# Kernel optimization log

Hardware: AMD Instinct MI355X
Metric: run time of the kernel (lower is better)

## Reference

```python
import jax, jax.numpy as jnp
import numpy as np

B, Z, TDIM, CF, A, R, T = 1024, 256, 512, 1024, 64, 128, 64

def _lstm_cell(x, h, c, Wih, Whh, b):
    # PyTorch gate order: i, f, g, o
    g = x @ Wih.T + h @ Whh.T + b
    i, f, gg, o = jnp.split(g, 4, axis=-1)
    c = jax.nn.sigmoid(f) * c + jax.nn.sigmoid(i) * jnp.tanh(gg)
    h = jax.nn.sigmoid(o) * jnp.tanh(c)
    return h, c

def setup_inputs() -> dict:
    key = jax.random.key(0)
    ks = jax.random.split(key, 24)
    s = lambda k, shape, fan: jax.random.normal(k, shape, jnp.float32) * (1.0 / np.sqrt(fan))
    d = {}
    d['z'] = jax.random.normal(ks[0], (B, Z), jnp.float32)
    d['z2t_w'] = s(ks[1], (TDIM, Z), Z)
    d['z2t_b'] = jnp.zeros((TDIM,), jnp.float32)
    in_a, in_r, in_t = TDIM + A, TDIM + A + R, TDIM + A + 1
    d['Wih_a'] = s(ks[2], (4 * CF, in_a), in_a); d['Whh_a'] = s(ks[3], (4 * CF, CF), CF); d['b_a'] = jnp.zeros((4 * CF,), jnp.float32)
    d['Wih_r'] = s(ks[4], (4 * CF, in_r), in_r); d['Whh_r'] = s(ks[5], (4 * CF, CF), CF); d['b_r'] = jnp.zeros((4 * CF,), jnp.float32)
    d['Wih_t'] = s(ks[6], (4 * CF, in_t), in_t); d['Whh_t'] = s(ks[7], (4 * CF, CF), CF); d['b_t'] = jnp.zeros((4 * CF,), jnp.float32)
    d['e2act_w'] = s(ks[8], (A, CF), CF); d['e2act_b'] = jnp.zeros((A,), jnp.float32)
    d['e2res_w'] = s(ks[9], (R, CF), CF); d['e2res_b'] = jnp.zeros((R,), jnp.float32)
    d['e2ts_w1'] = s(ks[10], (CF // 2, CF), CF); d['e2ts_b1'] = jnp.zeros((CF // 2,), jnp.float32)
    d['e2ts_w2'] = s(ks[11], (1, CF // 2), CF // 2); d['e2ts_b2'] = jnp.zeros((1,), jnp.float32)
    return d

def reference(z, z2t_w, z2t_b, Wih_a, Whh_a, b_a, Wih_r, Whh_r, b_r, Wih_t, Whh_t, b_t,
              e2act_w, e2act_b, e2res_w, e2res_b, e2ts_w1, e2ts_b1, e2ts_w2, e2ts_b2):
    t_rec = jax.nn.relu(z @ z2t_w.T + z2t_b)                  # [B, TDIM]
    b = t_rec.shape[0]
    act_oh = jnp.tile(jax.nn.one_hot(A - 1, A, dtype=jnp.float32), (b, 1))   # EOT activity
    res_oh = jnp.tile(jax.nn.one_hot(R - 1, R, dtype=jnp.float32), (b, 1))   # EOT resource
    ts_v = jnp.zeros((b, 1), jnp.float32)
    zeros_h = jnp.zeros((b, CF), jnp.float32)
    carry0 = (act_oh, res_oh, ts_v, zeros_h, zeros_h, zeros_h, zeros_h, zeros_h, zeros_h)

    def step(carry, _):
        act_oh, res_oh, ts_v, ha, ca, hr, cr, ht, ct = carry
        xa = jnp.concatenate([t_rec, act_oh], axis=-1)
        ha, ca = _lstm_cell(xa, ha, ca, Wih_a, Whh_a, b_a)
        act_logits = ha @ e2act_w.T + e2act_b                 # [B, A]
        act_oh2 = jax.nn.one_hot(jnp.argmax(act_logits, axis=-1), A, dtype=jnp.float32)
        xr = jnp.concatenate([t_rec, act_oh2, res_oh], axis=-1)
        hr, cr = _lstm_cell(xr, hr, cr, Wih_r, Whh_r, b_r)
        res_logits = hr @ e2res_w.T + e2res_b                 # [B, R]
        res_oh2 = jax.nn.one_hot(jnp.argmax(res_logits, axis=-1), R, dtype=jnp.float32)
        xt = jnp.concatenate([t_rec, act_oh2, ts_v], axis=-1)
        ht, ct = _lstm_cell(xt, ht, ct, Wih_t, Whh_t, b_t)
        ts_new = jax.nn.relu(ht @ e2ts_w1.T + e2ts_b1) @ e2ts_w2.T + e2ts_b2  # [B, 1]
        new_carry = (act_oh2, res_oh2, ts_new, ha, ca, hr, cr, ht, ct)
        return new_carry, (act_logits, res_logits, ts_new)

    _, (act_seq, res_seq, ts_seq) = jax.lax.scan(step, carry0, None, length=T)
    acts_rec = jax.nn.softmax(jnp.transpose(act_seq, (1, 0, 2)), axis=2)   # [B, T, A]
    ress_rec = jax.nn.softmax(jnp.transpose(res_seq, (1, 0, 2)), axis=2)   # [B, T, R]
    ts_rec = jnp.transpose(ts_seq[..., 0], (1, 0))                         # [B, T]
    return acts_rec, ts_rec, ress_rec
```

## Files before the change

kernel.cpp:

```cpp
#include <hip/hip_runtime.h>
#include <math.h>


__device__ __forceinline__ float sigf(float x) { return 1.0f / (1.0f + expf(-x)); }

typedef __attribute__((ext_vector_type(8))) _Float16 f16x8;
typedef __attribute__((ext_vector_type(4))) float f32x4;

__device__ __forceinline__ void split_f16(float x, unsigned short& hi, unsigned short& lo) {
    _Float16 h = (_Float16)x;
    float r = (x - (float)h) * 2048.0f;
    _Float16 l = (_Float16)r;
    hi = __builtin_bit_cast(unsigned short, h);
    lo = __builtin_bit_cast(unsigned short, l);
}

#define GLDS(gp, lp) __builtin_amdgcn_global_load_lds( \
    (const __attribute__((address_space(1))) void*)(gp), \
    (__attribute__((address_space(3))) void*)(lp), 16, 0, 0)

__global__ __launch_bounds__(256, 4) void step1(
    const unsigned short* __restrict__ Ah, const unsigned short* __restrict__ Al,
    const unsigned short* __restrict__ WA0, const unsigned short* __restrict__ WA1,
    const float* __restrict__ base_a, const float* __restrict__ Ea, const int* __restrict__ aidx,
    float* __restrict__ ca, unsigned short* __restrict__ oAh, unsigned short* __restrict__ oAl,
    float* __restrict__ haf,
    const unsigned short* __restrict__ Th, const unsigned short* __restrict__ Tl,
    const unsigned short* __restrict__ W10, const unsigned short* __restrict__ W11,
    const float* __restrict__ b1, float* __restrict__ u,
    const float* __restrict__ hrf, const float* __restrict__ resT4, const float* __restrict__ resb,
    float* __restrict__ out_res, int* __restrict__ ridx, int t, int Loff)
{
    int L = blockIdx.x + Loff;
    if (L >= 576) {
        if (t == 0) return;
        int lane = threadIdx.x & 63, w = threadIdx.x >> 6;
        int b = (L - 576) * 4 + w;
        float acc0 = resb[lane], acc1 = resb[lane + 64];
        const float4* arow = (const float4*)(hrf + (size_t)b * 1024);
#pragma unroll 4
        for (int k4 = 0; k4 < 256; k4++) {
            float4 a4 = arow[k4];
            float4 w40 = *(const float4*)(resT4 + ((size_t)k4 * 128 + lane) * 4);
            float4 w41 = *(const float4*)(resT4 + ((size_t)k4 * 128 + lane + 64) * 4);
            acc0 += a4.x * w40.x + a4.y * w40.y + a4.z * w40.z + a4.w * w40.w;
            acc1 += a4.x * w41.x + a4.y * w41.y + a4.z * w41.z + a4.w * w41.w;
        }
        float v = acc0; int idx = lane;
        if (acc1 > v) { v = acc1; idx = lane + 64; }
#pragma unroll
        for (int off = 32; off; off >>= 1) {
            float ov = __shfl_xor(v, off);
            int   oi = __shfl_xor(idx, off);
            if (ov > v || (ov == v && oi < idx)) { v = ov; idx = oi; }
        }
        float e0 = expf(acc0 - v), e1 = expf(acc1 - v);
        float s = e0 + e1;
#pragma unroll
        for (int off = 32; off; off >>= 1) s += __shfl_xor(s, off);
        float* dst = out_res + ((size_t)b * 64 + (t - 1)) * 128;
        dst[lane] = e0 / s; dst[lane + 64] = e1 / s;
        if (lane == 0) ridx[b] = idx;
        return;
    }

    __shared__ unsigned short lds[8192];
    const unsigned short *pAh, *pAl, *pWh, *pWl;
    int x, jy; bool isA;
    if (L < 512) {
        isA = true;
        int xcd = L & 7, idx = L >> 3;
        jy = xcd * 8 + (idx >> 3);
        x = idx & 7;
        pAh = Ah; pAl = Al; pWh = WA0; pWl = WA1;
    } else {
        isA = false;
        int t2 = L - 512;
        x = t2 & 7; jy = t2 >> 3;
        pAh = Th; pAl = Tl; pWh = W10; pWl = W11;
    }
    const int tid = threadIdx.x, wave = tid >> 6, lane = tid & 63;
    const int lrow = lane & 15, lq = lane >> 4;
    const int m0 = x * 128;

    f32x4 acch[2][4], accl[2][4];
#pragma unroll
    for (int i = 0; i < 2; i++)
#pragma unroll
        for (int j = 0; j < 4; j++) {
            acch[i][j] = (f32x4){0.f, 0.f, 0.f, 0.f};
            accl[i][j] = (f32x4){0.f, 0.f, 0.f, 0.f};
        }

    const int nrow = isA ? (wave * 1024 + jy * 16 + lrow) : (jy * 64 + wave * 16 + lrow);
    const size_t ar0 = (size_t)(m0 + (wave * 2 + 0) * 16 + lrow) * 1024 + lq * 8;
    const size_t ar1 = (size_t)(m0 + (wave * 2 + 1) * 16 + lrow) * 1024 + lq * 8;

    f16x8 ah[2][2], al[2][2];

    auto LOADA = [&](int it, int s) {
        int k = it * 32;
        ah[s][0] = *(const f16x8*)(pAh + ar0 + k);
        al[s][0] = *(const f16x8*)(pAl + ar0 + k);
        ah[s][1] = *(const f16x8*)(pAh + ar1 + k);
        al[s][1] = *(const f16x8*)(pAl + ar1 + k);
    };
    auto STAGEB = [&](int it, int p) {
        int k = it * 32 + lq * 8;
        unsigned short* bp = &lds[p * 4096];
        GLDS(pWh + (size_t)nrow * 1024 + k, bp + wave * 512);
        GLDS(pWl + (size_t)nrow * 1024 + k, bp + 2048 + wave * 512);
    };
    auto COMPUTE = [&](int s, int p) {
        unsigned short* bp = &lds[p * 4096];
#pragma unroll
        for (int nh = 0; nh < 2; nh++) {
            f16x8 bh[2], bl[2];
#pragma unroll
            for (int q = 0; q < 2; q++) {
                int ni = nh * 2 + q;
                bh[q] = *(const f16x8*)(bp + ni * 512 + lane * 8);
                bl[q] = *(const f16x8*)(bp + 2048 + ni * 512 + lane * 8);
            }
#pragma unroll
            for (int mi = 0; mi < 2; mi++)
#pragma unroll
                for (int q = 0; q < 2; q++) {
                    int ni = nh * 2 + q;
                    acch[mi][ni] = __builtin_amdgcn_mfma_f32_16x16x32_f16(ah[s][mi], bh[q], acch[mi][ni], 0, 0, 0);
                    accl[mi][ni] = __builtin_amdgcn_mfma_f32_16x16x32_f16(al[s][mi], bh[q], accl[mi][ni], 0, 0, 0);
                    accl[mi][ni] = __builtin_amdgcn_mfma_f32_16x16x32_f16(ah[s][mi], bl[q], accl[mi][ni], 0, 0, 0);
                }
        }
    };

    LOADA(0, 0);
    STAGEB(0, 0);
    for (int it = 0; it < 30; it += 2) {
        STAGEB(it + 1, 1);
        asm volatile("s_waitcnt vmcnt(2)" ::: "memory");
        __builtin_amdgcn_s_barrier();
        __builtin_amdgcn_sched_barrier(0);
        LOADA(it + 1, 1);
        COMPUTE(0, 0);
        __builtin_amdgcn_sched_barrier(0);
        __builtin_amdgcn_s_barrier();
        STAGEB(it + 2, 0);
        asm volatile("s_waitcnt vmcnt(2)" ::: "memory");
        __builtin_amdgcn_s_barrier();
        __builtin_amdgcn_sched_barrier(0);
        LOADA(it + 2, 0);
        COMPUTE(1, 1);
        __builtin_amdgcn_sched_barrier(0);
        __builtin_amdgcn_s_barrier();
    }
    STAGEB(31, 1);
    asm volatile("s_waitcnt vmcnt(2)" ::: "memory");
    __builtin_amdgcn_s_barrier();
    __builtin_amdgcn_sched_barrier(0);
    LOADA(31, 1);
    COMPUTE(0, 0);
    __builtin_amdgcn_sched_barrier(0);
    __builtin_amdgcn_s_barrier();
    asm volatile("s_waitcnt vmcnt(0)" ::: "memory");
    __builtin_amdgcn_s_barrier();
    __builtin_amdgcn_sched_barrier(0);
    COMPUTE(1, 1);

    const float s_lo = 1.0f / 2048.0f;
    if (isA) {
        int j = jy * 16 + lrow;
#pragma unroll
        for (int mi = 0; mi < 2; mi++)
#pragma unroll
            for (int r = 0; r < 4; r++) {
                int row = m0 + wave * 32 + mi * 16 + lq * 4 + r;
                size_t rb = (size_t)row * 4096 + j;
                const float* e1 = Ea + (size_t)aidx[row] * 4096 + j;
                float gi = acch[mi][0][r] + accl[mi][0][r] * s_lo + base_a[rb]        + e1[0];
                float gf = acch[mi][1][r] + accl[mi][1][r] * s_lo + base_a[rb + 1024] + e1[1024];
                float gg = acch[mi][2][r] + accl[mi][2][r] * s_lo + base_a[rb + 2048] + e1[2048];
                float go = acch[mi][3][r] + accl[mi][3][r] * s_lo + base_a[rb + 3072] + e1[3072];
                size_t ci = (size_t)row * 1024 + j;
                float cn = sigf(gf) * ca[ci] + sigf(gi) * tanhf(gg);
                ca[ci] = cn;
                float hn = sigf(go) * tanhf(cn);
                haf[ci] = hn;
                split_f16(hn, oAh[ci], oAl[ci]);
            }
    } else {
#pragma unroll
        for (int mi = 0; mi < 2; mi++)
#pragma unroll
            for (int ni = 0; ni < 4; ni++) {
                int col = jy * 64 + ni * 16 + lrow;
                float bv = b1[col];
#pragma unroll
                for (int r = 0; r < 4; r++) {
                    int row = m0 + wave * 32 + mi * 16 + lq * 4 + r;
                    float v = acch[mi][ni][r] + accl[mi][ni][r] * s_lo + bv;
                    u[(size_t)row * 512 + col] = fmaxf(v, 0.0f);
                }
            }
    }
}

__global__ __launch_bounds__(256, 4) void step3(
    const unsigned short* __restrict__ Rh, const unsigned short* __restrict__ Rl,
    const unsigned short* __restrict__ WR0, const unsigned short* __restrict__ WR1,
    const float* __restrict__ base_r, const float* __restrict__ Er_a, const float* __restrict__ Er_r,
    const int* __restrict__ aidx, const int* __restrict__ ridx, const float* __restrict__ tsv,
    float* __restrict__ cr, unsigned short* __restrict__ oRh, unsigned short* __restrict__ oRl,
    float* __restrict__ hrf,
    const unsigned short* __restrict__ Th, const unsigned short* __restrict__ Tl,
    const unsigned short* __restrict__ WT0, const unsigned short* __restrict__ WT1,
    const float* __restrict__ base_t, const float* __restrict__ Et_a, const float* __restrict__ wtts,
    float* __restrict__ ct, unsigned short* __restrict__ oTh, unsigned short* __restrict__ oTl)
{
    __shared__ unsigned short lds[8192];
    int L = blockIdx.x;
    int xcd = L & 7, idx = L >> 3;
    int g = xcd * 16 + (idx >> 3);
    int x = idx & 7;
    int z = g >> 6, jy = g & 63;
    const unsigned short* pAh = z ? Th : Rh;
    const unsigned short* pAl = z ? Tl : Rl;
    const unsigned short* pWh = z ? WT0 : WR0;
    const unsigned short* pWl = z ? WT1 : WR1;

    const int tid = threadIdx.x, wave = tid >> 6, lane = tid & 63;
    const int lrow = lane & 15, lq = lane >> 4;
    const int m0 = x * 128;

    f32x4 acch[2][4], accl[2][4];
#pragma unroll
    for (int i = 0; i < 2; i++)
#pragma unroll
        for (int j = 0; j < 4; j++) {
            acch[i][j] = (f32x4){0.f, 0.f, 0.f, 0.f};
            accl[i][j] = (f32x4){0.f, 0.f, 0.f, 0.f};
        }

    const int nrow = wave * 1024 + jy * 16 + lrow;
    const size_t ar0 = (size_t)(m0 + (wave * 2 + 0) * 16 + lrow) * 1024 + lq * 8;
    const size_t ar1 = (size_t)(m0 + (wave * 2 + 1) * 16 + lrow) * 1024 + lq * 8;

    f16x8 ah[2][2], al[2][2];

    auto LOADA = [&](int it, int s) {
        int k = it * 32;
        ah[s][0] = *(const f16x8*)(pAh + ar0 + k);
        al[s][0] = *(const f16x8*)(pAl + ar0 + k);
        ah[s][1] = *(const f16x8*)(pAh + ar1 + k);
        al[s][1] = *(const f16x8*)(pAl + ar1 + k);
    };
    auto STAGEB = [&](int it, int p) {
        int k = it * 32 + lq * 8;
        unsigned short* bp = &lds[p * 4096];
        GLDS(pWh + (size_t)nrow * 1024 + k, bp + wave * 512);
        GLDS(pWl + (size_t)nrow * 1024 + k, bp + 2048 + wave * 512);
    };
    auto COMPUTE = [&](int s, int p) {
        unsigned short* bp = &lds[p * 4096];
#pragma unroll
        for (int nh = 0; nh < 2; nh++) {
            f16x8 bh[2], bl[2];
#pragma unroll
            for (int q = 0; q < 2; q++) {
                int ni = nh * 2 + q;
                bh[q] = *(const f16x8*)(bp + ni * 512 + lane * 8);
                bl[q] = *(const f16x8*)(bp + 2048 + ni * 512 + lane * 8);
            }
#pragma unroll
            for (int mi = 0; mi < 2; mi++)
#pragma unroll
                for (int q = 0; q < 2; q++) {
                    int ni = nh * 2 + q;
                    acch[mi][ni] = __builtin_amdgcn_mfma_f32_16x16x32_f16(ah[s][mi], bh[q], acch[mi][ni], 0, 0, 0);
                    accl[mi][ni] = __builtin_amdgcn_mfma_f32_16x16x32_f16(al[s][mi], bh[q], accl[mi][ni], 0, 0, 0);
                    accl[mi][ni] = __builtin_amdgcn_mfma_f32_16x16x32_f16(ah[s][mi], bl[q], accl[mi][ni], 0, 0, 0);
                }
        }
    };

    LOADA(0, 0);
    STAGEB(0, 0);
    for (int it = 0; it < 30; it += 2) {
        STAGEB(it + 1, 1);
        asm volatile("s_waitcnt vmcnt(2)" ::: "memory");
        __builtin_amdgcn_s_barrier();
        __builtin_amdgcn_sched_barrier(0);
        LOADA(it + 1, 1);
        COMPUTE(0, 0);
        __builtin_amdgcn_sched_barrier(0);
        __builtin_amdgcn_s_barrier();
        STAGEB(it + 2, 0);
        asm volatile("s_waitcnt vmcnt(2)" ::: "memory");
        __builtin_amdgcn_s_barrier();
        __builtin_amdgcn_sched_barrier(0);
        LOADA(it + 2, 0);
        COMPUTE(1, 1);
        __builtin_amdgcn_sched_barrier(0);
        __builtin_amdgcn_s_barrier();
    }
    STAGEB(31, 1);
    asm volatile("s_waitcnt vmcnt(2)" ::: "memory");
    __builtin_amdgcn_s_barrier();
    __builtin_amdgcn_sched_barrier(0);
    LOADA(31, 1);
    COMPUTE(0, 0);
    __builtin_amdgcn_sched_barrier(0);
    __builtin_amdgcn_s_barrier();
    asm volatile("s_waitcnt vmcnt(0)" ::: "memory");
    __builtin_amdgcn_s_barrier();
    __builtin_amdgcn_sched_barrier(0);
    COMPUTE(1, 1);

    const float s_lo = 1.0f / 2048.0f;
    const int j = jy * 16 + lrow;
    if (z == 0) {
#pragma unroll
        for (int mi = 0; mi < 2; mi++)
#pragma unroll
            for (int r = 0; r < 4; r++) {
                int row = m0 + wave * 32 + mi * 16 + lq * 4 + r;
                size_t rb = (size_t)row * 4096 + j;
                const float* e1 = Er_a + (size_t)aidx[row] * 4096 + j;
                const float* e2 = Er_r + (size_t)ridx[row] * 4096 + j;
                float gi = acch[mi][0][r] + accl[mi][0][r] * s_lo + base_r[rb]        + e1[0]    + e2[0];
                float gf = acch[mi][1][r] + accl[mi][1][r] * s_lo + base_r[rb + 1024] + e1[1024] + e2[1024];
                float gg = acch[mi][2][r] + accl[mi][2][r] * s_lo + base_r[rb + 2048] + e1[2048] + e2[2048];
                float go = acch[mi][3][r] + accl[mi][3][r] * s_lo + base_r[rb + 3072] + e1[3072] + e2[3072];
                size_t ci = (size_t)row * 1024 + j;
                float cn = sigf(gf) * cr[ci] + sigf(gi) * tanhf(gg);
                cr[ci] = cn;
                float hn = sigf(go) * tanhf(cn);
                hrf[ci] = hn;
                split_f16(hn, oRh[ci], oRl[ci]);
            }
    } else {
#pragma unroll
        for (int mi = 0; mi < 2; mi++)
#pragma unroll
            for (int r = 0; r < 4; r++) {
                int row = m0 + wave * 32 + mi * 16 + lq * 4 + r;
                size_t rb = (size_t)row * 4096 + j;
                const float* e1 = Et_a + (size_t)aidx[row] * 4096 + j;
                float tv = tsv[row];
                float gi = acch[mi][0][r] + accl[mi][0][r] * s_lo + base_t[rb]        + e1[0];
                float gf = acch[mi][1][r] + accl[mi][1][r] * s_lo + base_t[rb + 1024] + e1[1024];
                float gg = acch[mi][2][r] + accl[mi][2][r] * s_lo + base_t[rb + 2048] + e1[2048];
                float go = acch[mi][3][r] + accl[mi][3][r] * s_lo + base_t[rb + 3072] + e1[3072];
                gi = fmaf(tv, wtts[j], gi);        gf = fmaf(tv, wtts[j + 1024], gf);
                gg = fmaf(tv, wtts[j + 2048], gg); go = fmaf(tv, wtts[j + 3072], go);
                size_t ci = (size_t)row * 1024 + j;
                float cn = sigf(gf) * ct[ci] + sigf(gi) * tanhf(gg);
                ct[ci] = cn;
                float hn = sigf(go) * tanhf(cn);
                split_f16(hn, oTh[ci], oTl[ci]);
            }
    }
}

__global__ __launch_bounds__(256) void heads(
    const float* __restrict__ haf, const float* __restrict__ actT4, const float* __restrict__ actb,
    float* __restrict__ out_acts, int* __restrict__ aidx, int tact,
    const float* __restrict__ u, const float* __restrict__ w2, const float* __restrict__ b2,
    float* __restrict__ out_ts, float* __restrict__ tsv, int tts)
{
    int blk = blockIdx.x;
    int lane = threadIdx.x & 63, w = threadIdx.x >> 6;
    if (blk < 256) {
        if (tact < 0) return;
        int b = blk * 4 + w;
        float acc = actb[lane];
        const float4* arow = (const float4*)(haf + (size_t)b * 1024);
#pragma unroll 4
        for (int k4 = 0; k4 < 256; k4++) {
            float4 a4 = arow[k4];
            float4 w4 = *(const float4*)(actT4 + ((size_t)k4 * 64 + lane) * 4);
            acc += a4.x * w4.x + a4.y * w4.y + a4.z * w4.z + a4.w * w4.w;
        }
        float v = acc; int idx = lane;
#pragma unroll
        for (int off = 32; off; off >>= 1) {
            float ov = __shfl_xor(v, off);
            int   oi = __shfl_xor(idx, off);
            if (ov > v || (ov == v && oi < idx)) { v = ov; idx = oi; }
        }
        float e = expf(acc - v);
        float s = e;
#pragma unroll
        for (int off = 32; off; off >>= 1) s += __shfl_xor(s, off);
        out_acts[((size_t)b * 64 + tact) * 64 + lane] = e / s;
        if (lane == 0) aidx[b] = idx;
    } else {
        if (tts < 0) return;
        int b = (blk - 256) * 4 + w;
        const float* ur = u + (size_t)b * 512;
        float s = 0.0f;
#pragma unroll
        for (int q = 0; q < 8; q++) s = fmaf(ur[lane + q * 64], w2[lane + q * 64], s);
#pragma unroll
        for (int off = 32; off; off >>= 1) s += __shfl_xor(s, off);
        if (lane == 0) {
            float r = s + b2[0];
            out_ts[b * 64 + tts] = r;
            tsv[b] = r;
        }
    }
}

__global__ __launch_bounds__(256) void gemm_f32(
    const float* __restrict__ A0, const float* __restrict__ W0, float* __restrict__ C0,
    const float* __restrict__ A1, const float* __restrict__ W1, float* __restrict__ C1,
    int lda, int ldw, int ldc, int K, const float* __restrict__ bias, int relu)
{
    const float* Ap = blockIdx.z ? A1 : A0;
    const float* Wp = blockIdx.z ? W1 : W0;
    float*       Cp = blockIdx.z ? C1 : C0;
    __shared__ float As[16][128];
    __shared__ float Bs[16][64];
    const int tid = threadIdx.x;
    const int m0 = blockIdx.x * 128, n0 = blockIdx.y * 64;
    const int tx = tid & 7, ty = tid >> 3;
    const bool wal = (ldw & 3) == 0;
    float acc[4][8];
#pragma unroll
    for (int i = 0; i < 4; i++)
#pragma unroll
        for (int j = 0; j < 8; j++) acc[i][j] = 0.0f;

    for (int k0 = 0; k0 < K; k0 += 16) {
        __syncthreads();
#pragma unroll
        for (int q = 0; q < 2; q++) {
            int t2 = tid + q * 256;
            int kq = t2 & 3, m = t2 >> 2;
            float4 v = *(const float4*)(Ap + (size_t)(m0 + m) * lda + k0 + kq * 4);
            As[kq * 4 + 0][m] = v.x; As[kq * 4 + 1][m] = v.y;
            As[kq * 4 + 2][m] = v.z; As[kq * 4 + 3][m] = v.w;
        }
        {
            int kq = tid & 3, n = tid >> 2;
            const float* src = Wp + (size_t)(n0 + n) * ldw + k0 + kq * 4;
            float4 v;
            if (wal) v = *(const float4*)src;
            else { v.x = src[0]; v.y = src[1]; v.z = src[2]; v.w = src[3]; }
            Bs[kq * 4 + 0][n] = v.x; Bs[kq * 4 + 1][n] = v.y;
            Bs[kq * 4 + 2][n] = v.z; Bs[kq * 4 + 3][n] = v.w;
        }
        __syncthreads();
#pragma unroll
        for (int k = 0; k < 16; k++) {
            float a4[4], b8[8];
            *(float4*)a4 = *(const float4*)&As[k][ty * 4];
            *(float4*)(b8) = *(const float4*)&Bs[k][tx * 8];
            *(float4*)(b8 + 4) = *(const float4*)&Bs[k][tx * 8 + 4];
#pragma unroll
            for (int i = 0; i < 4; i++)
#pragma unroll
                for (int j = 0; j < 8; j++) acc[i][j] = fmaf(a4[i], b8[j], acc[i][j]);
        }
    }
#pragma unroll
    for (int i = 0; i < 4; i++) {
        int m = m0 + ty * 4 + i;
        float vb[8];
#pragma unroll
        for (int j = 0; j < 8; j++) {
            float v = acc[i][j];
            if (bias) v += bias[n0 + tx * 8 + j];
            if (relu) v = fmaxf(v, 0.0f);
            vb[j] = v;
        }
        float* dst = Cp + (size_t)m * ldc + n0 + tx * 8;
        *(float4*)dst = make_float4(vb[0], vb[1], vb[2], vb[3]);
        *(float4*)(dst + 4) = make_float4(vb[4], vb[5], vb[6], vb[7]);
    }
}

__global__ void extract_cols(const float* __restrict__ Wih, int ldw, int col0, int ncols,
                             float* __restrict__ E)
{
    int i = blockIdx.x * 256 + threadIdx.x;
    if (i >= ncols * 4096) return;
    int c = i % ncols, j = i / ncols;
    E[(size_t)c * 4096 + j] = Wih[(size_t)j * ldw + col0 + c];
}

__global__ void split_mat_h(const float* __restrict__ X,
                            unsigned short* __restrict__ hi, unsigned short* __restrict__ lo, int n)
{
    int i = blockIdx.x * 256 + threadIdx.x;
    if (i >= n) return;
    split_f16(X[i], hi[i], lo[i]);
}

__global__ void transpose_pack(const float* __restrict__ W, int K, int C, float* __restrict__ out)
{
    int i = blockIdx.x * 256 + threadIdx.x;
    if (i >= C * K) return;
    int c = i / K, k = i - c * K;
    out[(((size_t)(k >> 2) * C + c) << 2) + (k & 3)] = W[i];
}

__global__ void init_state(float* __restrict__ cc, unsigned int* __restrict__ hilo,
                           float* __restrict__ tsv, int* __restrict__ aidx, int* __restrict__ ridx)
{
    int i = blockIdx.x * 256 + threadIdx.x;
    if (i < 3 * 1024 * 1024) cc[i] = 0.0f;
    if (i < 6 * 1024 * 1024) hilo[i] = 0u;
    if (i < 1024) { tsv[i] = 0.0f; aidx[i] = 63; ridx[i] = 127; }
}

extern "C" void kernel_launch(void* const* d_in, const int* in_sizes, int n_in,
                              void* d_out, int out_size, void* d_ws, size_t ws_size,
                              hipStream_t stream)
{
    const float* z       = (const float*)d_in[0];
    const float* z2t_w   = (const float*)d_in[1];
    const float* z2t_b   = (const float*)d_in[2];
    const float* Wih_a   = (const float*)d_in[3];
    const float* Whh_a   = (const float*)d_in[4];
    const float* b_a     = (const float*)d_in[5];
    const float* Wih_r   = (const float*)d_in[6];
    const float* Whh_r   = (const float*)d_in[7];
    const float* b_r     = (const float*)d_in[8];
    const float* Wih_t   = (const float*)d_in[9];
    const float* Whh_t   = (const float*)d_in[10];
    const float* b_t     = (const float*)d_in[11];
    const float* e2act_w = (const float*)d_in[12];
    const float* e2act_b = (const float*)d_in[13];
    const float* e2res_w = (const float*)d_in[14];
    const float* e2res_b = (const float*)d_in[15];
    const float* e2ts_w1 = (const float*)d_in[16];
    const float* e2ts_b1 = (const float*)d_in[17];
    const float* e2ts_w2 = (const float*)d_in[18];
    const float* e2ts_b2 = (const float*)d_in[19];

    float* out_acts = (float*)d_out;
    float* out_ts   = out_acts + (size_t)1024 * 64 * 64;
    float* out_res  = out_ts + 1024 * 64;

    float* ws = (float*)d_ws;
    size_t off = 0;
    auto alloc = [&](size_t n) { float* p = ws + off; off += n; return p; };
    float* t_rec  = alloc((size_t)1024 * 512);
    float* base_a = alloc((size_t)1024 * 4096);
    float* base_r = alloc((size_t)1024 * 4096);
    float* base_t = alloc((size_t)1024 * 4096);
    float* Ea     = alloc((size_t)64 * 4096);
    float* Er_a   = alloc((size_t)64 * 4096);
    float* Er_r   = alloc((size_t)128 * 4096);
    float* Et_a   = alloc((size_t)64 * 4096);
    float* wtts   = alloc(4096);
    float* cc     = alloc((size_t)3 * 1024 * 1024);
    float* ca = cc, * cr = cc + 1048576, * ct = cc + 2097152;
    float* haf    = alloc((size_t)1024 * 1024);
    float* hrf    = alloc((size_t)1024 * 1024);
    float* u      = alloc((size_t)1024 * 512);
    float* tsv    = alloc(1024);
    int*   aidx   = (int*)alloc(1024);
    int*   ridx   = (int*)alloc(1024);
    float* actT4  = alloc((size_t)64 * 1024);
    float* resT4  = alloc((size_t)128 * 1024);
    unsigned short* hilo = (unsigned short*)alloc((size_t)6 * 1024 * 1024);
    const size_t U = 1048576;
    unsigned short* haSp0[2] = {hilo,         hilo + U};
    unsigned short* haSp1[2] = {hilo + 2 * U, hilo + 3 * U};
    unsigned short* hrSp0[2] = {hilo + 4 * U, hilo + 5 * U};
    unsigned short* hrSp1[2] = {hilo + 6 * U, hilo + 7 * U};
    unsigned short* htSp0[2] = {hilo + 8 * U, hilo + 9 * U};
    unsigned short* htSp1[2] = {hilo + 10 * U, hilo + 11 * U};
    unsigned short* WA0 = (unsigned short*)alloc((size_t)2 * 1024 * 1024);
    unsigned short* WA1 = (unsigned short*)alloc((size_t)2 * 1024 * 1024);
    unsigned short* WR0 = (unsigned short*)alloc((size_t)2 * 1024 * 1024);
    unsigned short* WR1 = (unsigned short*)alloc((size_t)2 * 1024 * 1024);
    unsigned short* WT0 = (unsigned short*)alloc((size_t)2 * 1024 * 1024);
    unsigned short* WT1 = (unsigned short*)alloc((size_t)2 * 1024 * 1024);
    unsigned short* W10 = (unsigned short*)alloc((size_t)256 * 1024);
    unsigned short* W11 = (unsigned short*)alloc((size_t)256 * 1024);

    dim3 blk(256);
    init_state<<<(6 * 1024 * 1024 + 255) / 256, blk, 0, stream>>>(cc, (unsigned int*)hilo, tsv, aidx, ridx);

    gemm_f32<<<dim3(8, 8, 1), blk, 0, stream>>>(z, z2t_w, t_rec, z, z2t_w, t_rec,
                                                256, 256, 512, 256, z2t_b, 1);
    gemm_f32<<<dim3(8, 64, 1), blk, 0, stream>>>(t_rec, Wih_a, base_a, t_rec, Wih_a, base_a,
                                                 512, 576, 4096, 512, b_a, 0);
    gemm_f32<<<dim3(8, 64, 1), blk, 0, stream>>>(t_rec, Wih_r, base_r, t_rec, Wih_r, base_r,
                                                 512, 704, 4096, 512, b_r, 0);
    gemm_f32<<<dim3(8, 64, 1), blk, 0, stream>>>(t_rec, Wih_t, base_t, t_rec, Wih_t, base_t,
                                                 512, 577, 4096, 512, b_t, 0);
    extract_cols<<<(64 * 4096 + 255) / 256, blk, 0, stream>>>(Wih_a, 576, 512, 64, Ea);
    extract_cols<<<(64 * 4096 + 255) / 256, blk, 0, stream>>>(Wih_r, 704, 512, 64, Er_a);
    extract_cols<<<(128 * 4096 + 255) / 256, blk, 0, stream>>>(Wih_r, 704, 576, 128, Er_r);
    extract_cols<<<(64 * 4096 + 255) / 256, blk, 0, stream>>>(Wih_t, 577, 512, 64, Et_a);
    extract_cols<<<(4096 + 255) / 256, blk, 0, stream>>>(Wih_t, 577, 576, 1, wtts);
    transpose_pack<<<(64 * 1024 + 255) / 256, blk, 0, stream>>>(e2act_w, 1024, 64, actT4);
    transpose_pack<<<(128 * 1024 + 255) / 256, blk, 0, stream>>>(e2res_w, 1024, 128, resT4);
    split_mat_h<<<(4194304 + 255) / 256, blk, 0, stream>>>(Whh_a, WA0, WA1, 4194304);
    split_mat_h<<<(4194304 + 255) / 256, blk, 0, stream>>>(Whh_r, WR0, WR1, 4194304);
    split_mat_h<<<(4194304 + 255) / 256, blk, 0, stream>>>(Whh_t, WT0, WT1, 4194304);
    split_mat_h<<<(524288 + 255) / 256, blk, 0, stream>>>(e2ts_w1, W10, W11, 524288);

    for (int t = 0; t < 64; t++) {
        int rd = t & 1, wr = rd ^ 1;
        step1<<<832, blk, 0, stream>>>(
            haSp0[rd], haSp1[rd], WA0, WA1, base_a, Ea, aidx,
            ca, haSp0[wr], haSp1[wr], haf,
            htSp0[rd], htSp1[rd], W10, W11, e2ts_b1, u,
            hrf, resT4, e2res_b, out_res, ridx, t, 0);
        heads<<<512, blk, 0, stream>>>(haf, actT4, e2act_b, out_acts, aidx, t,
                                       u, e2ts_w2, e2ts_b2, out_ts, tsv, t - 1);
        step3<<<1024, blk, 0, stream>>>(
            hrSp0[rd], hrSp1[rd], WR0, WR1, base_r, Er_a, Er_r, aidx, ridx, tsv,
            cr, hrSp0[wr], hrSp1[wr], hrf,
            htSp0[rd], htSp1[rd], WT0, WT1, base_t, Et_a, wtts,
            ct, htSp0[wr], htSp1[wr]);
    }
    step1<<<320, blk, 0, stream>>>(
        haSp0[0], haSp1[0], WA0, WA1, base_a, Ea, aidx,
        ca, haSp0[1], haSp1[1], haf,
        htSp0[0], htSp1[0], W10, W11, e2ts_b1, u,
        hrf, resT4, e2res_b, out_res, ridx, 64, 512);
    heads<<<512, blk, 0, stream>>>(haf, actT4, e2act_b, out_acts, aidx, -1,
                                   u, e2ts_w2, e2ts_b2, out_ts, tsv, 63);
}
```

Measured before the change: 14.29 ms.

## Double workgroup size to 512 threads with 2x wider N tile per block

The recurrent LSTM GEMM kernels now run 8 waves per block arranged as a 4x2 grid. Each block covers twice as many N columns while keeping 128 rows of M, so the A operand loaded per block is reused across both N halves, and the block count is halved. The LDS staging buffers double in size, the XCD-aware block remapping is dropped in favour of a plain linear mapping, and the response head path now handles 8 batch rows per block. In exchange, per-block LDS and register pressure rise and the grid is smaller, which may reduce occupancy and L2 locality across XCDs.

```diff
diff --git a/kernel.cpp b/kernel.cpp
--- a/kernel.cpp
+++ b/kernel.cpp
@@ -19,7 +19,7 @@
     (const __attribute__((address_space(1))) void*)(gp), \
     (__attribute__((address_space(3))) void*)(lp), 16, 0, 0)
 
-__global__ __launch_bounds__(256, 4) void step1(
+__global__ __launch_bounds__(512, 4) void step1(
     const unsigned short* __restrict__ Ah, const unsigned short* __restrict__ Al,
     const unsigned short* __restrict__ WA0, const unsigned short* __restrict__ WA1,
     const float* __restrict__ base_a, const float* __restrict__ Ea, const int* __restrict__ aidx,
@@ -32,10 +32,10 @@
     float* __restrict__ out_res, int* __restrict__ ridx, int t, int Loff)
 {
     int L = blockIdx.x + Loff;
-    if (L >= 576) {
+    if (L >= 288) {
         if (t == 0) return;
         int lane = threadIdx.x & 63, w = threadIdx.x >> 6;
-        int b = (L - 576) * 4 + w;
+        int b = (L - 288) * 8 + w;
         float acc0 = resb[lane], acc1 = resb[lane + 64];
         const float4* arow = (const float4*)(hrf + (size_t)b * 1024);
 #pragma unroll 4
@@ -64,22 +64,22 @@
         return;
     }
 
-    __shared__ unsigned short lds[8192];
+    __shared__ unsigned short lds[16384];
     const unsigned short *pAh, *pAl, *pWh, *pWl;
     int x, jy; bool isA;
-    if (L < 512) {
+    if (L < 256) {
         isA = true;
-        int xcd = L & 7, idx = L >> 3;
-        jy = xcd * 8 + (idx >> 3);
-        x = idx & 7;
+        x = L & 7;
+        jy = L >> 3;
         pAh = Ah; pAl = Al; pWh = WA0; pWl = WA1;
     } else {
         isA = false;
-        int t2 = L - 512;
+        int t2 = L - 256;
         x = t2 & 7; jy = t2 >> 3;
         pAh = Th; pAl = Tl; pWh = W10; pWl = W11;
     }
     const int tid = threadIdx.x, wave = tid >> 6, lane = tid & 63;
+    const int wm = wave >> 1, wn = wave & 1;
     const int lrow = lane & 15, lq = lane >> 4;
     const int m0 = x * 128;
 
@@ -92,9 +92,10 @@
             accl[i][j] = (f32x4){0.f, 0.f, 0.f, 0.f};
         }
 
-    const int nrow = isA ? (wave * 1024 + jy * 16 + lrow) : (jy * 64 + wave * 16 + lrow);
-    const size_t ar0 = (size_t)(m0 + (wave * 2 + 0) * 16 + lrow) * 1024 + lq * 8;
-    const size_t ar1 = (size_t)(m0 + (wave * 2 + 1) * 16 + lrow) * 1024 + lq * 8;
+    const int nrow = isA ? ((wave >> 1) * 1024 + jy * 32 + (wave & 1) * 16 + lrow)
+                         : (jy * 128 + (wave & 1) * 64 + (wave >> 1) * 16 + lrow);
+    const size_t ar0 = (size_t)(m0 + (wm * 2 + 0) * 16 + lrow) * 1024 + lq * 8;
+    const size_t ar1 = (size_t)(m0 + (wm * 2 + 1) * 16 + lrow) * 1024 + lq * 8;
 
     f16x8 ah[2][2], al[2][2];
 
@@ -107,20 +108,20 @@
     };
     auto STAGEB = [&](int it, int p) {
         int k = it * 32 + lq * 8;
-        unsigned short* bp = &lds[p * 4096];
+        unsigned short* bp = &lds[p * 8192];
         GLDS(pWh + (size_t)nrow * 1024 + k, bp + wave * 512);
-        GLDS(pWl + (size_t)nrow * 1024 + k, bp + 2048 + wave * 512);
+        GLDS(pWl + (size_t)nrow * 1024 + k, bp + 4096 + wave * 512);
     };
     auto COMPUTE = [&](int s, int p) {
-        unsigned short* bp = &lds[p * 4096];
+        unsigned short* bp = &lds[p * 8192];
 #pragma unroll
         for (int nh = 0; nh < 2; nh++) {
             f16x8 bh[2], bl[2];
 #pragma unroll
             for (int q = 0; q < 2; q++) {
                 int ni = nh * 2 + q;
-                bh[q] = *(const f16x8*)(bp + ni * 512 + lane * 8);
-                bl[q] = *(const f16x8*)(bp + 2048 + ni * 512 + lane * 8);
+                bh[q] = *(const f16x8*)(bp + (ni * 2 + wn) * 512 + lane * 8);
+                bl[q] = *(const f16x8*)(bp + 4096 + (ni * 2 + wn) * 512 + lane * 8);
             }
 #pragma unroll
             for (int mi = 0; mi < 2; mi++)
@@ -169,12 +170,12 @@
 
     const float s_lo = 1.0f / 2048.0f;
     if (isA) {
-        int j = jy * 16 + lrow;
+        int j = jy * 32 + wn * 16 + lrow;
 #pragma unroll
         for (int mi = 0; mi < 2; mi++)
 #pragma unroll
             for (int r = 0; r < 4; r++) {
-                int row = m0 + wave * 32 + mi * 16 + lq * 4 + r;
+                int row = m0 + wm * 32 + mi * 16 + lq * 4 + r;
                 size_t rb = (size_t)row * 4096 + j;
                 const float* e1 = Ea + (size_t)aidx[row] * 4096 + j;
                 float gi = acch[mi][0][r] + accl[mi][0][r] * s_lo + base_a[rb]        + e1[0];
@@ -193,11 +194,11 @@
         for (int mi = 0; mi < 2; mi++)
 #pragma unroll
             for (int ni = 0; ni < 4; ni++) {
-                int col = jy * 64 + ni * 16 + lrow;
+                int col = jy * 128 + wn * 64 + ni * 16 + lrow;
                 float bv = b1[col];
 #pragma unroll
                 for (int r = 0; r < 4; r++) {
-                    int row = m0 + wave * 32 + mi * 16 + lq * 4 + r;
+                    int row = m0 + wm * 32 + mi * 16 + lq * 4 + r;
                     float v = acch[mi][ni][r] + accl[mi][ni][r] * s_lo + bv;
                     u[(size_t)row * 512 + col] = fmaxf(v, 0.0f);
                 }
@@ -205,7 +206,7 @@
     }
 }
 
-__global__ __launch_bounds__(256, 4) void step3(
+__global__ __launch_bounds__(512, 4) void step3(
     const unsigned short* __restrict__ Rh, const unsigned short* __restrict__ Rl,
     const unsigned short* __restrict__ WR0, const unsigned short* __restrict__ WR1,
     const float* __restrict__ base_r, const float* __restrict__ Er_a, const float* __restrict__ Er_r,
@@ -217,18 +218,18 @@
     const float* __restrict__ base_t, const float* __restrict__ Et_a, const float* __restrict__ wtts,
     float* __restrict__ ct, unsigned short* __restrict__ oTh, unsigned short* __restrict__ oTl)
 {
-    __shared__ unsigned short lds[8192];
+    __shared__ unsigned short lds[16384];
     int L = blockIdx.x;
-    int xcd = L & 7, idx = L >> 3;
-    int g = xcd * 16 + (idx >> 3);
-    int x = idx & 7;
-    int z = g >> 6, jy = g & 63;
+    int z = L >> 8;
+    int r8 = L & 255;
+    int x = r8 & 7, jy = r8 >> 3;
     const unsigned short* pAh = z ? Th : Rh;
     const unsigned short* pAl = z ? Tl : Rl;
     const unsigned short* pWh = z ? WT0 : WR0;
     const unsigned short* pWl = z ? WT1 : WR1;
 
     const int tid = threadIdx.x, wave = tid >> 6, lane = tid & 63;
+    const int wm = wave >> 1, wn = wave & 1;
     const int lrow = lane & 15, lq = lane >> 4;
     const int m0 = x * 128;
 
@@ -241,9 +242,9 @@
             accl[i][j] = (f32x4){0.f, 0.f, 0.f, 0.f};
         }
 
-    const int nrow = wave * 1024 + jy * 16 + lrow;
-    const size_t ar0 = (size_t)(m0 + (wave * 2 + 0) * 16 + lrow) * 1024 + lq * 8;
-    const size_t ar1 = (size_t)(m0 + (wave * 2 + 1) * 16 + lrow) * 1024 + lq * 8;
+    const int nrow = (wave >> 1) * 1024 + jy * 32 + (wave & 1) * 16 + lrow;
+    const size_t ar0 = (size_t)(m0 + (wm * 2 + 0) * 16 + lrow) * 1024 + lq * 8;
+    const size_t ar1 = (size_t)(m0 + (wm * 2 + 1) * 16 + lrow) * 1024 + lq * 8;
 
     f16x8 ah[2][2], al[2][2];
 
@@ -256,20 +257,20 @@
     };
     auto STAGEB = [&](int it, int p) {
         int k = it * 32 + lq * 8;
-        unsigned short* bp = &lds[p * 4096];
+        unsigned short* bp = &lds[p * 8192];
         GLDS(pWh + (size_t)nrow * 1024 + k, bp + wave * 512);
-        GLDS(pWl + (size_t)nrow * 1024 + k, bp + 2048 + wave * 512);
+        GLDS(pWl + (size_t)nrow * 1024 + k, bp + 4096 + wave * 512);
     };
     auto COMPUTE = [&](int s, int p) {
-        unsigned short* bp = &lds[p * 4096];
+        unsigned short* bp = &lds[p * 8192];
 #pragma unroll
         for (int nh = 0; nh < 2; nh++) {
             f16x8 bh[2], bl[2];
 #pragma unroll
             for (int q = 0; q < 2; q++) {
                 int ni = nh * 2 + q;
-                bh[q] = *(const f16x8*)(bp + ni * 512 + lane * 8);
-                bl[q] = *(const f16x8*)(bp + 2048 + ni * 512 + lane * 8);
+                bh[q] = *(const f16x8*)(bp + (ni * 2 + wn) * 512 + lane * 8);
+                bl[q] = *(const f16x8*)(bp + 4096 + (ni * 2 + wn) * 512 + lane * 8);
             }
 #pragma unroll
             for (int mi = 0; mi < 2; mi++)
@@ -317,13 +318,13 @@
     COMPUTE(1, 1);
 
     const float s_lo = 1.0f / 2048.0f;
-    const int j = jy * 16 + lrow;
+    const int j = jy * 32 + wn * 16 + lrow;
     if (z == 0) {
 #pragma unroll
         for (int mi = 0; mi < 2; mi++)
 #pragma unroll
             for (int r = 0; r < 4; r++) {
-                int row = m0 + wave * 32 + mi * 16 + lq * 4 + r;
+                int row = m0 + wm * 32 + mi * 16 + lq * 4 + r;
                 size_t rb = (size_t)row * 4096 + j;
                 const float* e1 = Er_a + (size_t)aidx[row] * 4096 + j;
                 const float* e2 = Er_r + (size_t)ridx[row] * 4096 + j;
@@ -343,7 +344,7 @@
         for (int mi = 0; mi < 2; mi++)
 #pragma unroll
             for (int r = 0; r < 4; r++) {
-                int row = m0 + wave * 32 + mi * 16 + lq * 4 + r;
+                int row = m0 + wm * 32 + mi * 16 + lq * 4 + r;
                 size_t rb = (size_t)row * 4096 + j;
                 const float* e1 = Et_a + (size_t)aidx[row] * 4096 + j;
                 float tv = tsv[row];
@@ -583,6 +584,7 @@
     unsigned short* W11 = (unsigned short*)alloc((size_t)256 * 1024);
 
     dim3 blk(256);
+    dim3 blk512(512);
     init_state<<<(6 * 1024 * 1024 + 255) / 256, blk, 0, stream>>>(cc, (unsigned int*)hilo, tsv, aidx, ridx);
 
     gemm_f32<<<dim3(8, 8, 1), blk, 0, stream>>>(z, z2t_w, t_rec, z, z2t_w, t_rec,
@@ -607,24 +609,24 @@
 
     for (int t = 0; t < 64; t++) {
         int rd = t & 1, wr = rd ^ 1;
-        step1<<<832, blk, 0, stream>>>(
+        step1<<<416, blk512, 0, stream>>>(
             haSp0[rd], haSp1[rd], WA0, WA1, base_a, Ea, aidx,
             ca, haSp0[wr], haSp1[wr], haf,
             htSp0[rd], htSp1[rd], W10, W11, e2ts_b1, u,
             hrf, resT4, e2res_b, out_res, ridx, t, 0);
         heads<<<512, blk, 0, stream>>>(haf, actT4, e2act_b, out_acts, aidx, t,
                                        u, e2ts_w2, e2ts_b2, out_ts, tsv, t - 1);
-        step3<<<1024, blk, 0, stream>>>(
+        step3<<<512, blk512, 0, stream>>>(
             hrSp0[rd], hrSp1[rd], WR0, WR1, base_r, Er_a, Er_r, aidx, ridx, tsv,
             cr, hrSp0[wr], hrSp1[wr], hrf,
             htSp0[rd], htSp1[rd], WT0, WT1, base_t, Et_a, wtts,
             ct, htSp0[wr], htSp1[wr]);
     }
-    step1<<<320, blk, 0, stream>>>(
+    step1<<<160, blk512, 0, stream>>>(
         haSp0[0], haSp1[0], WA0, WA1, base_a, Ea, aidx,
         ca, haSp0[1], haSp1[1], haf,
         htSp0[0], htSp1[0], W10, W11, e2ts_b1, u,
-        hrf, resT4, e2res_b, out_res, ridx, 64, 512);
+        hrf, resT4, e2res_b, out_res, ridx, 64, 256);
     heads<<<512, blk, 0, stream>>>(haf, actT4, e2act_b, out_acts, aidx, -1,
                                    u, e2ts_w2, e2ts_b2, out_ts, tsv, 63);
 }
```

Result: no change. 14.40 ms (+0.8%).
